# Kernel optimization log

Hardware: AMD Instinct MI355X
Metric: run time of the kernel (lower is better)

The kernel has to match this reference:

```python
import jax, jax.numpy as jnp
import numpy as np

NUM_HEADS = 8


def setup_inputs() -> dict:
    key = jax.random.key(0)
    k1, k2 = jax.random.split(key)
    B, N, C = 2, 8192, 512
    x = jax.random.normal(k1, (B, N, C), dtype=jnp.float32)
    # torch nn.Linear weight layout: [out_features, in_features]
    W_qkv = jax.random.normal(k2, (3 * C, C), dtype=jnp.float32) * (C ** -0.5)
    return {"x": x, "W_qkv": W_qkv}


def reference(x, W_qkv):
    B, N, C = x.shape
    H = NUM_HEADS
    d = C // H
    scale = d ** -0.5

    # qkv projection (no bias): [B, N, 3C]
    qkv = x @ W_qkv.T
    # [B, N, 3, H, d] -> [3, B, H, N, d]
    qkv = qkv.reshape(B, N, 3, H, d).transpose(2, 0, 3, 1, 4)
    q, k, v = qkv[0], qkv[1], qkv[2]

    # mean-center keys over sequence dim
    k_hat = k - jnp.mean(k, axis=2, keepdims=True)          # [B, H, N, d]

    # KV aggregation: g = k_hat^T @ v  -> [B, H, d, d]
    g = jnp.einsum('bhnd,bhne->bhde', k_hat, v)

    # k_sum over sequence (numerically ~0 since k_hat is centered, kept faithful)
    k_sum = jnp.sum(k_hat, axis=2)                          # [B, H, d]
    q_ksum = jnp.einsum('bhnd,bhd->bhn', q, k_sum)[..., None]  # [B, H, N, 1]

    # denominator: N*scale + q @ k_sum^T
    t_D = N * scale + q_ksum                                # [B, H, N, 1]
    # numerator: scale + q @ g (broadcast of ones*scale over last dim)
    T_N = scale + jnp.einsum('bhnd,bhde->bhne', q, g)       # [B, H, N, d]

    z = T_N / t_D                                           # [B, H, N, d]
    return z
```

## Files before the change

### kernel.cpp

```cpp
#include <hip/hip_runtime.h>

typedef unsigned short u16;
typedef unsigned int u32;
typedef __attribute__((ext_vector_type(8))) short short8;
typedef __attribute__((ext_vector_type(4))) float f32x4;
typedef __attribute__((ext_vector_type(4))) unsigned short ushort4v;
typedef __attribute__((ext_vector_type(4))) float float4v;

__device__ __forceinline__ float bf2f(u16 u) {
    return __uint_as_float(((u32)u) << 16);
}
__device__ __forceinline__ u16 f2bf(float f) {
    u32 u = __float_as_uint(f);
    u += 0x7FFF + ((u >> 16) & 1);
    return (u16)(u >> 16);
}
__device__ __forceinline__ short8 cvt8(float4 a, float4 b) {
    short8 r;
    r[0] = (short)f2bf(a.x); r[1] = (short)f2bf(a.y);
    r[2] = (short)f2bf(a.z); r[3] = (short)f2bf(a.w);
    r[4] = (short)f2bf(b.x); r[5] = (short)f2bf(b.y);
    r[6] = (short)f2bf(b.z); r[7] = (short)f2bf(b.w);
    return r;
}
__device__ __forceinline__ void stage16(const u16* g, u16* l) {
    __builtin_amdgcn_global_load_lds(
        (const __attribute__((address_space(1))) unsigned int*)g,
        (__attribute__((address_space(3))) unsigned int*)l, 16, 0, 0);
}

__global__ __launch_bounds__(256) void cvt_t(const float* __restrict__ x,
                                             u16* __restrict__ xT,
                                             u16* __restrict__ xb,
                                             float* __restrict__ sp2,
                                             const float* __restrict__ W,
                                             u16* __restrict__ wvb) {
    const int bid = blockIdx.x;
    const int t = threadIdx.x;
    if (bid >= 1024) {
        const int i = (bid - 1024) * 256 + t;
        float4v v = ((const float4v*)(W + 524288))[i];
        ushort4v r;
        r[0] = f2bf(v[0]); r[1] = f2bf(v[1]); r[2] = f2bf(v[2]); r[3] = f2bf(v[3]);
        ((ushort4v*)wvb)[i] = r;
        return;
    }
    __shared__ u16 tile[64][136];
    const int ct = bid & 3, nt = (bid >> 2) & 127, b = bid >> 9;
    const int r = t >> 2, c0 = (t & 3) * 32;
    const float* src = x + ((size_t)(b * 8192 + nt * 64 + r)) * 512 + ct * 128 + c0;
    short8 r8[4];
#pragma unroll
    for (int j = 0; j < 8; j += 2) {
        float4 v0 = *(const float4*)(src + j * 4);
        float4 v1 = *(const float4*)(src + j * 4 + 4);
        r8[j >> 1] = cvt8(v0, v1);
        *(short8*)(&tile[r][c0 + j * 4]) = r8[j >> 1];
    }
    u16* xbrow = xb + ((size_t)(b * 8192 + nt * 64 + r)) * 512 + ct * 128 + c0;
#pragma unroll
    for (int jj = 0; jj < 4; ++jj) *(short8*)(xbrow + jj * 8) = r8[jj];
    __syncthreads();
    const int c = t >> 1, half = t & 1;
    u16 vals[32];
    float psum = 0.f;
#pragma unroll
    for (int i = 0; i < 32; ++i) {
        vals[i] = tile[half * 32 + i][c];
        psum += bf2f(vals[i]);
    }
    u16* dst = xT + ((size_t)(b * 512 + ct * 128 + c)) * 8192 + nt * 64 + half * 32;
#pragma unroll
    for (int j = 0; j < 4; ++j)
        *(int4*)(dst + j * 8) = *(int4*)(&vals[j * 8]);
    psum += __shfl_xor(psum, 1);
    if ((t & 1) == 0)
        sp2[((size_t)(b * 128 + nt)) * 512 + ct * 128 + c] = psum;
}

template <int STRIDE, int KLEN>
__device__ __forceinline__ void gemm_core(const u16* __restrict__ Ag,
                                          const u16* __restrict__ Bg,
                                          u16* As, u16* Bs, int t,
                                          f32x4 acc[4][4]) {
    const int wv = t >> 6, l = t & 63;
    const int lr = l & 15, lk = (l >> 4) * 8;
    const int wm = (wv >> 1) * 64, wn = (wv & 1) * 64;
    const int srow = l >> 2, scol = (l & 3) * 8;

    u16* Ad0 = As + (wv * 32) * 32;
    u16* Ad1 = As + (wv * 32 + 16) * 32;
    u16* Bd0 = Bs + (wv * 32) * 32;
    u16* Bd1 = Bs + (wv * 32 + 16) * 32;
    const u16* As0 = Ag + (size_t)(wv * 32 + srow) * STRIDE + scol;
    const u16* As1 = Ag + (size_t)(wv * 32 + 16 + srow) * STRIDE + scol;
    const u16* Bs0 = Bg + (size_t)(wv * 32 + srow) * STRIDE + scol;
    const u16* Bs1 = Bg + (size_t)(wv * 32 + 16 + srow) * STRIDE + scol;

    for (int k0 = 0; k0 < KLEN; k0 += 32) {
        stage16(As0 + k0, Ad0);
        stage16(As1 + k0, Ad1);
        stage16(Bs0 + k0, Bd0);
        stage16(Bs1 + k0, Bd1);
        __syncthreads();
        short8 af[4], bfr[4];
#pragma unroll
        for (int mi = 0; mi < 4; ++mi)
            af[mi] = *(const short8*)(As + (wm + mi * 16 + lr) * 32 + lk);
#pragma unroll
        for (int ni = 0; ni < 4; ++ni)
            bfr[ni] = *(const short8*)(Bs + (wn + ni * 16 + lr) * 32 + lk);
#pragma unroll
        for (int mi = 0; mi < 4; ++mi)
#pragma unroll
            for (int ni = 0; ni < 4; ++ni)
                acc[mi][ni] = __builtin_amdgcn_mfma_f32_16x16x32_bf16(
                    af[mi], bfr[ni], acc[mi][ni], 0, 0, 0);
        __syncthreads();
    }
}

__global__ __launch_bounds__(256) void syrk(const u16* __restrict__ xT,
                                            u16* __restrict__ Spart,
                                            const float* __restrict__ sp2,
                                            float* __restrict__ ssum) {
    const int bid = blockIdx.x, t = threadIdx.x;
    if (bid >= 512) {
        const int idx = (bid - 512) * 256 + t;
        const int b = idx >> 9, c = idx & 511;
        float a = 0.f;
        for (int j = 0; j < 128; ++j) a += sp2[(size_t)(b * 128 + j) * 512 + c];
        ssum[idx] = a;
        return;
    }
    __shared__ u16 As[128 * 32];
    __shared__ u16 Bs[128 * 32];
    const int nt = bid & 3, mt = (bid >> 2) & 3;
    const int ks = (bid >> 4) & 15, b = bid >> 8;
    const u16* Ag = xT + ((size_t)(b * 512 + mt * 128)) * 8192 + ks * 512;
    const u16* Bg = xT + ((size_t)(b * 512 + nt * 128)) * 8192 + ks * 512;

    f32x4 zz = {0.f, 0.f, 0.f, 0.f};
    f32x4 acc[4][4];
    for (int i = 0; i < 4; ++i)
        for (int j = 0; j < 4; ++j) acc[i][j] = zz;

    gemm_core<8192, 512>(Ag, Bg, As, Bs, t, acc);

    const int l = t & 63, wv = t >> 6;
    const int lr = l & 15;
    const int wm = (wv >> 1) * 64, wn = (wv & 1) * 64;
    u16* out = Spart + ((size_t)(b * 16 + ks)) * 262144;
#pragma unroll
    for (int mi = 0; mi < 4; ++mi)
#pragma unroll
        for (int ni = 0; ni < 4; ++ni) {
            int col = nt * 128 + wn + ni * 16 + lr;
#pragma unroll
            for (int j = 0; j < 4; ++j) {
                int row = mt * 128 + wm + mi * 16 + (l >> 4) * 4 + j;
                out[(size_t)row * 512 + col] = f2bf(acc[mi][ni][j]);
            }
        }
}

__global__ __launch_bounds__(256) void reduceS(const u16* __restrict__ Spart,
                                               const float* __restrict__ s,
                                               u16* __restrict__ Sbf) {
    const int b = blockIdx.x >> 9, m = blockIdx.x & 511;
    const int t = threadIdx.x;
    const float sm = s[b * 512 + m] * (1.0f / 8192.0f);
#pragma unroll
    for (int rep = 0; rep < 2; ++rep) {
        const int n = rep * 256 + t;
        float acc = 0.f;
#pragma unroll
        for (int ks = 0; ks < 16; ++ks)
            acc += bf2f(Spart[((size_t)(b * 16 + ks)) * 262144 + (size_t)m * 512 + n]);
        acc -= sm * s[b * 512 + n];
        Sbf[(size_t)b * 262144 + (size_t)m * 512 + n] = f2bf(acc);
    }
}

__global__ __launch_bounds__(256) void pgemm(const u16* __restrict__ wvb,
                                             const u16* __restrict__ Sbf,
                                             u16* __restrict__ Pb) {
    __shared__ u16 As[128 * 32];
    __shared__ u16 Bs[128 * 32];
    const int t = threadIdx.x;
    const int nt = blockIdx.x & 3, mt = (blockIdx.x >> 2) & 3, b = blockIdx.x >> 4;
    const u16* Ag = wvb + (size_t)(mt * 128) * 512;
    const u16* Bg = Sbf + (size_t)b * 262144 + (size_t)(nt * 128) * 512;

    f32x4 zz = {0.f, 0.f, 0.f, 0.f};
    f32x4 acc[4][4];
    for (int i = 0; i < 4; ++i)
        for (int j = 0; j < 4; ++j) acc[i][j] = zz;

    gemm_core<512, 512>(Ag, Bg, As, Bs, t, acc);

    const int l = t & 63, wv = t >> 6;
    const int lr = l & 15;
    const int wm = (wv >> 1) * 64, wn = (wv & 1) * 64;
    u16* out = Pb + (size_t)b * 262144;
#pragma unroll
    for (int mi = 0; mi < 4; ++mi)
#pragma unroll
        for (int ni = 0; ni < 4; ++ni) {
            int col = nt * 128 + wn + ni * 16 + lr;
#pragma unroll
            for (int j = 0; j < 4; ++j) {
                int row = mt * 128 + wm + mi * 16 + (l >> 4) * 4 + j;
                out[(size_t)row * 512 + col] = f2bf(acc[mi][ni][j]);
            }
        }
}

__global__ __launch_bounds__(256) void g2(const float* __restrict__ W,
                                          const u16* __restrict__ Pb,
                                          float* __restrict__ gfull) {
    const int bh = blockIdx.x >> 2, nt = blockIdx.x & 3;
    const int b = bh >> 3, h = bh & 7;
    const int t = threadIdx.x, w = t >> 6, l = t & 63;
    const int lr = l & 15, lk = (l >> 4) * 8;
    const float* Wk = W + (size_t)(512 + h * 64 + w * 16 + lr) * 512;
    const u16* Pr = Pb + (size_t)b * 262144 + (size_t)(h * 64 + nt * 16 + lr) * 512;

    f32x4 acc = {0.f, 0.f, 0.f, 0.f};
    for (int k0 = 0; k0 < 512; k0 += 32) {
        short8 af = cvt8(*(const float4*)(Wk + k0 + lk),
                         *(const float4*)(Wk + k0 + lk + 4));
        short8 bfr = *(const short8*)(Pr + k0 + lk);
        acc = __builtin_amdgcn_mfma_f32_16x16x32_bf16(af, bfr, acc, 0, 0, 0);
    }
#pragma unroll
    for (int j = 0; j < 4; ++j) {
        int d = w * 16 + (l >> 4) * 4 + j;
        int e = nt * 16 + lr;
        gfull[(size_t)bh * 4096 + d * 64 + e] = acc[j];
    }
}

__global__ __launch_bounds__(256) void fold(const float* __restrict__ gfull,
                                            const float* __restrict__ W,
                                            u16* __restrict__ Wgb) {
    const int bh = blockIdx.x >> 3, cb = blockIdx.x & 7;
    const int b = bh >> 3, h = bh & 7;
    const int t = threadIdx.x;
    __shared__ float gs[4096];
    for (int i = t; i < 4096; i += 256) gs[i] = gfull[bh * 4096 + i];
    __syncthreads();
    const int c = cb * 64 + (t & 63);
    const int eg = (t >> 6) * 16;
    float acc[16];
#pragma unroll
    for (int j = 0; j < 16; ++j) acc[j] = 0.f;
    for (int d = 0; d < 64; ++d) {
        float w = W[(size_t)(h * 64 + d) * 512 + c];
#pragma unroll
        for (int j = 0; j < 16; ++j) acc[j] += w * gs[d * 64 + eg + j];
    }
#pragma unroll
    for (int j = 0; j < 16; ++j)
        Wgb[(size_t)(b * 512 + h * 64 + eg + j) * 512 + c] = f2bf(acc[j]);
}

__global__ __launch_bounds__(256) void out_z(const u16* __restrict__ xb,
                                             const u16* __restrict__ Wgb,
                                             float* __restrict__ z) {
    __shared__ u16 As[128 * 32];
    __shared__ u16 Bs[128 * 32];
    const int t = threadIdx.x;
    const int m0 = blockIdx.x * 128;
    const int b = blockIdx.x >> 6;
    const int n0 = blockIdx.y * 128;

    f32x4 zz = {0.f, 0.f, 0.f, 0.f};
    f32x4 acc[4][4];
    for (int i = 0; i < 4; ++i)
        for (int j = 0; j < 4; ++j) acc[i][j] = zz;

    gemm_core<512, 512>(xb + (size_t)m0 * 512,
                        Wgb + (size_t)b * 262144 + (size_t)n0 * 512, As, Bs, t, acc);

    const int l = t & 63, wv = t >> 6;
    const int lr = l & 15;
    const int wm = (wv >> 1) * 64, wn = (wv & 1) * 64;
#pragma unroll
    for (int mi = 0; mi < 4; ++mi)
#pragma unroll
        for (int ni = 0; ni < 4; ++ni) {
            int he = n0 + wn + ni * 16 + lr;
            int h = he >> 6, e = he & 63;
#pragma unroll
            for (int j = 0; j < 4; ++j) {
                int row = m0 + wm + mi * 16 + (l >> 4) * 4 + j;
                int nidx = row & 8191;
                z[((size_t)(b * 8 + h) * 8192 + nidx) * 64 + e] =
                    (acc[mi][ni][j] + 0.125f) * 0.0009765625f;
            }
        }
}

extern "C" void kernel_launch(void* const* d_in, const int* in_sizes, int n_in,
                              void* d_out, int out_size, void* d_ws, size_t ws_size,
                              hipStream_t stream) {
    const float* x = (const float*)d_in[0];
    const float* W = (const float*)d_in[1];
    float* z = (float*)d_out;

    char* ws = (char*)d_ws;
    u16* xT      = (u16*)(ws);
    u16* xb      = (u16*)(ws + 16777216);
    u16* Spart   = (u16*)(ws + 33554432);
    u16* Sbf     = (u16*)(ws + 50331648);
    float* sp2   = (float*)(ws + 51380224);
    float* ssum  = (float*)(ws + 51904512);
    u16* wvb     = (u16*)(ws + 51908608);
    u16* Pb      = (u16*)(ws + 52432896);
    float* gfull = (float*)(ws + 53481472);
    u16* Wgb     = (u16*)(ws + 53743616);

    cvt_t<<<1280, 256, 0, stream>>>(x, xT, xb, sp2, W, wvb);
    syrk<<<516, 256, 0, stream>>>(xT, Spart, sp2, ssum);
    reduceS<<<1024, 256, 0, stream>>>(Spart, ssum, Sbf);
    pgemm<<<32, 256, 0, stream>>>(wvb, Sbf, Pb);
    g2<<<64, 256, 0, stream>>>(W, Pb, gfull);
    fold<<<128, 256, 0, stream>>>(gfull, W, Wgb);
    out_z<<<dim3(128, 4), 256, 0, stream>>>(xb, Wgb, z);
}
```

Measured before the change: 91.15 us.

## Precompute per-head Wq^T·Wk product and fuse g2+fold into one MFMA GEMM

Adds extra blocks to the conversion kernel that compute a per-head product U = Wq_h^T · Wk_h in bf16, which is independent of x. This lets the separate g2 and fold kernels, which read fp32 W and ran a scalar fp32 fold loop, be replaced by a single LDS-staged MFMA GEMM (Pb × U) that writes Wgb directly. It removes one kernel launch and the gfull round trip. The cost is an extra bf16 rounding of the intermediate U and a larger 512x512-per-head GEMM in the wgg kernel.

```diff
diff --git a/kernel.cpp b/kernel.cpp
--- a/kernel.cpp
+++ b/kernel.cpp
@@ -34,9 +34,65 @@
                                              u16* __restrict__ xb,
                                              float* __restrict__ sp2,
                                              const float* __restrict__ W,
-                                             u16* __restrict__ wvb) {
+                                             u16* __restrict__ wvb,
+                                             u16* __restrict__ Ub) {
+    __shared__ __align__(16) char smem[36864];
     const int bid = blockIdx.x;
     const int t = threadIdx.x;
+    if (bid >= 1280) {
+        const int u = bid - 1280;
+        const int h = u >> 4, mt = (u >> 2) & 3, ntt = u & 3;
+        u16 (*At)[72] = (u16(*)[72])smem;
+        u16 (*Bt)[72] = (u16(*)[72])(smem + 18432);
+        const int d = t >> 2, cg = (t & 3) * 32;
+        const float* wq = W + (size_t)(h * 64 + d) * 512 + mt * 128 + cg;
+        const float* wk = W + (size_t)(512 + h * 64 + d) * 512 + ntt * 128 + cg;
+#pragma unroll
+        for (int j = 0; j < 32; j += 4) {
+            float4 a = *(const float4*)(wq + j);
+            float4 kk = *(const float4*)(wk + j);
+            At[cg + j + 0][d] = f2bf(a.x); At[cg + j + 1][d] = f2bf(a.y);
+            At[cg + j + 2][d] = f2bf(a.z); At[cg + j + 3][d] = f2bf(a.w);
+            Bt[cg + j + 0][d] = f2bf(kk.x); Bt[cg + j + 1][d] = f2bf(kk.y);
+            Bt[cg + j + 2][d] = f2bf(kk.z); Bt[cg + j + 3][d] = f2bf(kk.w);
+        }
+        __syncthreads();
+        const int l = t & 63, wv = t >> 6;
+        const int lr = l & 15, lk = (l >> 4) * 8;
+        const int wm = (wv >> 1) * 64, wn = (wv & 1) * 64;
+        f32x4 zz = {0.f, 0.f, 0.f, 0.f};
+        f32x4 acc[4][4];
+        for (int i = 0; i < 4; ++i)
+            for (int j = 0; j < 4; ++j) acc[i][j] = zz;
+#pragma unroll
+        for (int k0 = 0; k0 < 64; k0 += 32) {
+            short8 af[4], bfr[4];
+#pragma unroll
+            for (int mi = 0; mi < 4; ++mi)
+                af[mi] = *(const short8*)(&At[wm + mi * 16 + lr][k0 + lk]);
+#pragma unroll
+            for (int ni = 0; ni < 4; ++ni)
+                bfr[ni] = *(const short8*)(&Bt[wn + ni * 16 + lr][k0 + lk]);
+#pragma unroll
+            for (int mi = 0; mi < 4; ++mi)
+#pragma unroll
+                for (int ni = 0; ni < 4; ++ni)
+                    acc[mi][ni] = __builtin_amdgcn_mfma_f32_16x16x32_bf16(
+                        af[mi], bfr[ni], acc[mi][ni], 0, 0, 0);
+        }
+#pragma unroll
+        for (int mi = 0; mi < 4; ++mi)
+#pragma unroll
+            for (int ni = 0; ni < 4; ++ni) {
+                int col = ntt * 128 + wn + ni * 16 + lr;
+#pragma unroll
+                for (int j = 0; j < 4; ++j) {
+                    int row = mt * 128 + wm + mi * 16 + (l >> 4) * 4 + j;
+                    Ub[((size_t)(h * 512 + row)) * 512 + col] = f2bf(acc[mi][ni][j]);
+                }
+            }
+        return;
+    }
     if (bid >= 1024) {
         const int i = (bid - 1024) * 256 + t;
         float4v v = ((const float4v*)(W + 524288))[i];
@@ -45,7 +101,7 @@
         ((ushort4v*)wvb)[i] = r;
         return;
     }
-    __shared__ u16 tile[64][136];
+    u16 (*tile)[136] = (u16(*)[136])smem;
     const int ct = bid & 3, nt = (bid >> 2) & 127, b = bid >> 9;
     const int r = t >> 2, c0 = (t & 3) * 32;
     const float* src = x + ((size_t)(b * 8192 + nt * 64 + r)) * 512 + ct * 128 + c0;
@@ -216,53 +272,63 @@
         }
 }
 
-__global__ __launch_bounds__(256) void g2(const float* __restrict__ W,
-                                          const u16* __restrict__ Pb,
-                                          float* __restrict__ gfull) {
-    const int bh = blockIdx.x >> 2, nt = blockIdx.x & 3;
+__global__ __launch_bounds__(256) void wgg(const u16* __restrict__ Ub,
+                                           const u16* __restrict__ Pb,
+                                           u16* __restrict__ Wgb) {
+    __shared__ u16 As[64 * 32];
+    __shared__ u16 Bs[128 * 32];
+    const int bh = blockIdx.x >> 2, ct = blockIdx.x & 3;
     const int b = bh >> 3, h = bh & 7;
-    const int t = threadIdx.x, w = t >> 6, l = t & 63;
+    const int t = threadIdx.x, wv = t >> 6, l = t & 63;
     const int lr = l & 15, lk = (l >> 4) * 8;
-    const float* Wk = W + (size_t)(512 + h * 64 + w * 16 + lr) * 512;
-    const u16* Pr = Pb + (size_t)b * 262144 + (size_t)(h * 64 + nt * 16 + lr) * 512;
-
-    f32x4 acc = {0.f, 0.f, 0.f, 0.f};
+    const int wm = (wv >> 1) * 32, wn = (wv & 1) * 64;
+    const int srow = l >> 2, scol = (l & 3) * 8;
+
+    const u16* Ag = Pb + (size_t)b * 262144 + (size_t)(h * 64) * 512;
+    const u16* Bg = Ub + (size_t)(h * 512 + ct * 128) * 512;
+    u16* Ad = As + (wv * 16) * 32;
+    u16* Bd0 = Bs + (wv * 32) * 32;
+    u16* Bd1 = Bs + (wv * 32 + 16) * 32;
+    const u16* As0 = Ag + (size_t)(wv * 16 + srow) * 512 + scol;
+    const u16* Bs0 = Bg + (size_t)(wv * 32 + srow) * 512 + scol;
+    const u16* Bs1 = Bg + (size_t)(wv * 32 + 16 + srow) * 512 + scol;
+
+    f32x4 zz = {0.f, 0.f, 0.f, 0.f};
+    f32x4 acc[2][4];
+    for (int i = 0; i < 2; ++i)
+        for (int j = 0; j < 4; ++j) acc[i][j] = zz;
+
     for (int k0 = 0; k0 < 512; k0 += 32) {
-        short8 af = cvt8(*(const float4*)(Wk + k0 + lk),
-                         *(const float4*)(Wk + k0 + lk + 4));
-        short8 bfr = *(const short8*)(Pr + k0 + lk);
-        acc = __builtin_amdgcn_mfma_f32_16x16x32_bf16(af, bfr, acc, 0, 0, 0);
-    }
-#pragma unroll
-    for (int j = 0; j < 4; ++j) {
-        int d = w * 16 + (l >> 4) * 4 + j;
-        int e = nt * 16 + lr;
-        gfull[(size_t)bh * 4096 + d * 64 + e] = acc[j];
-    }
-}
-
-__global__ __launch_bounds__(256) void fold(const float* __restrict__ gfull,
-                                            const float* __restrict__ W,
-                                            u16* __restrict__ Wgb) {
-    const int bh = blockIdx.x >> 3, cb = blockIdx.x & 7;
-    const int b = bh >> 3, h = bh & 7;
-    const int t = threadIdx.x;
-    __shared__ float gs[4096];
-    for (int i = t; i < 4096; i += 256) gs[i] = gfull[bh * 4096 + i];
-    __syncthreads();
-    const int c = cb * 64 + (t & 63);
-    const int eg = (t >> 6) * 16;
-    float acc[16];
-#pragma unroll
-    for (int j = 0; j < 16; ++j) acc[j] = 0.f;
-    for (int d = 0; d < 64; ++d) {
-        float w = W[(size_t)(h * 64 + d) * 512 + c];
-#pragma unroll
-        for (int j = 0; j < 16; ++j) acc[j] += w * gs[d * 64 + eg + j];
-    }
-#pragma unroll
-    for (int j = 0; j < 16; ++j)
-        Wgb[(size_t)(b * 512 + h * 64 + eg + j) * 512 + c] = f2bf(acc[j]);
+        stage16(As0 + k0, Ad);
+        stage16(Bs0 + k0, Bd0);
+        stage16(Bs1 + k0, Bd1);
+        __syncthreads();
+        short8 af[2], bfr[4];
+#pragma unroll
+        for (int mi = 0; mi < 2; ++mi)
+            af[mi] = *(const short8*)(As + (wm + mi * 16 + lr) * 32 + lk);
+#pragma unroll
+        for (int ni = 0; ni < 4; ++ni)
+            bfr[ni] = *(const short8*)(Bs + (wn + ni * 16 + lr) * 32 + lk);
+#pragma unroll
+        for (int mi = 0; mi < 2; ++mi)
+#pragma unroll
+            for (int ni = 0; ni < 4; ++ni)
+                acc[mi][ni] = __builtin_amdgcn_mfma_f32_16x16x32_bf16(
+                    af[mi], bfr[ni], acc[mi][ni], 0, 0, 0);
+        __syncthreads();
+    }
+#pragma unroll
+    for (int mi = 0; mi < 2; ++mi)
+#pragma unroll
+        for (int ni = 0; ni < 4; ++ni) {
+            int col = ct * 128 + wn + ni * 16 + lr;
+#pragma unroll
+            for (int j = 0; j < 4; ++j) {
+                int row = wm + mi * 16 + (l >> 4) * 4 + j;
+                Wgb[((size_t)(b * 512 + h * 64 + row)) * 512 + col] = f2bf(acc[mi][ni][j]);
+            }
+        }
 }
 
 __global__ __launch_bounds__(256) void out_z(const u16* __restrict__ xb,
@@ -318,14 +384,13 @@
     float* ssum  = (float*)(ws + 51904512);
     u16* wvb     = (u16*)(ws + 51908608);
     u16* Pb      = (u16*)(ws + 52432896);
-    float* gfull = (float*)(ws + 53481472);
-    u16* Wgb     = (u16*)(ws + 53743616);
-
-    cvt_t<<<1280, 256, 0, stream>>>(x, xT, xb, sp2, W, wvb);
+    u16* Ub      = (u16*)(ws + 53481472);
+    u16* Wgb     = (u16*)(ws + 57675776);
+
+    cvt_t<<<1408, 256, 0, stream>>>(x, xT, xb, sp2, W, wvb, Ub);
     syrk<<<516, 256, 0, stream>>>(xT, Spart, sp2, ssum);
     reduceS<<<1024, 256, 0, stream>>>(Spart, ssum, Sbf);
     pgemm<<<32, 256, 0, stream>>>(wvb, Sbf, Pb);
-    g2<<<64, 256, 0, stream>>>(W, Pb, gfull);
-    fold<<<128, 256, 0, stream>>>(gfull, W, Wgb);
+    wgg<<<64, 256, 0, stream>>>(Ub, Pb, Wgb);
     out_z<<<dim3(128, 4), 256, 0, stream>>>(xb, Wgb, z);
 }
```

Result: faster. 85.34 us (-6.4%).
